# Optimization experiments

Measured on AMD Instinct MI355X. Metric: run time of the kernel, lower is better.

The kernel has to match this reference:

```python
import jax, jax.numpy as jnp
import numpy as np
from jax import lax

B, C, H, W = 8, 19, 512, 512
LOW_T, HIGH_T = 100.0, 200.0  # cv2.Canny(img, 100, 200)
MAX_HYST_ITERS = 256          # safety cap on hysteresis fixed-point iterations

_KX = jnp.array([[-1., 0., 1.], [-2., 0., 2.], [-1., 0., 1.]], jnp.float32)
_KY = jnp.array([[-1., -2., -1.], [0., 0., 0.], [1., 2., 1.]], jnp.float32)


def _conv3(x, k):
    # x: [B, H+2, W+2] (already padded), k: [3,3] -> [B, H, W]
    return lax.conv_general_dilated(x[:, None], k[None, None], (1, 1), 'VALID')[:, 0]


def _dilate3(s):
    # 8-connected boolean dilation via 3x3 max window
    return lax.reduce_window(s.astype(jnp.int32), 0, lax.max, (1, 3, 3), (1, 1, 1), 'SAME') > 0


def _canny(img):
    # img: [B, H, W] float values in [0, 255]. Returns float32 edge map in {0,1}.
    b, h, w = img.shape
    pad = jnp.pad(img, ((0, 0), (1, 1), (1, 1)), mode='edge')
    gx = _conv3(pad, _KX)
    gy = _conv3(pad, _KY)
    mag = jnp.abs(gx) + jnp.abs(gy)  # cv2 default L1 gradient magnitude
    ang = jnp.degrees(jnp.arctan2(gy, gx)) % 180.0
    mp = jnp.pad(mag, ((0, 0), (1, 1), (1, 1)))
    nb = lambda dy, dx: mp[:, 1 + dy:1 + dy + h, 1 + dx:1 + dx + w]
    # non-maximum suppression along quantized gradient direction
    d0 = (ang < 22.5) | (ang >= 157.5)
    d45 = (ang >= 22.5) & (ang < 67.5)
    d90 = (ang >= 67.5) & (ang < 112.5)
    keep0 = (mag >= nb(0, 1)) & (mag >= nb(0, -1))
    keep45 = (mag >= nb(-1, 1)) & (mag >= nb(1, -1))
    keep90 = (mag >= nb(1, 0)) & (mag >= nb(-1, 0))
    keep135 = (mag >= nb(-1, -1)) & (mag >= nb(1, 1))
    keep = jnp.where(d0, keep0, jnp.where(d45, keep45, jnp.where(d90, keep90, keep135)))
    strong = keep & (mag > HIGH_T)
    weak = keep & (mag > LOW_T)  # weak includes strong
    # hysteresis: propagate strong labels through weak pixels to fixed point
    def cond(c):
        s, changed, it = c
        return changed & (it < MAX_HYST_ITERS)
    def body(c):
        s, _, it = c
        s2 = (weak & _dilate3(s)) | strong
        return (s2, jnp.any(s2 != s), it + 1)
    edges, _, _ = lax.while_loop(cond, body, (strong, jnp.array(True), jnp.array(0)))
    return edges.astype(jnp.float32)


def setup_inputs() -> dict:
    key = jax.random.key(0)
    k1, k2 = jax.random.split(key)
    pred = jax.random.normal(k1, (B, C, H, W), dtype=jnp.float32)
    labels = jax.random.uniform(k2, (B, H, W), dtype=jnp.float32)
    return {'pred': pred, 'labels': labels}


def reference(pred, labels):
    # pred_convert: per-pixel argmax over channel dim -> class ids [B, H, W]
    cls = jnp.argmax(pred, axis=1)
    # canny(): (img * 255).astype('uint8') -- class ids wrap mod 256
    img_p = ((cls * 255) % 256).astype(jnp.float32)
    # labels in [0,1): uint8 cast truncates toward zero
    img_l = jnp.floor(labels * 255.0)
    ep = _canny(img_p)  # [B, H, W] in {0,1}
    el = _canny(img_l)  # [B, H, W] in {0,1}
    # nn.CrossEntropyLoss() on float target of same shape: input [N=B, C=H, d1=W],
    # target is class probabilities; mean over N and d1.
    logp = jax.nn.log_softmax(ep, axis=1)
    return jnp.mean(jnp.sum(-el * logp, axis=1))
```

## Files before the change

kernel.cpp:

```cpp
#include <hip/hip_runtime.h>
#include <hip/hip_bf16.h>
#include <math.h>

typedef unsigned long long u64;
typedef unsigned char u8;
typedef unsigned short u16;
typedef unsigned int u32;

#define BB 8
#define CC 19
#define HH 512
#define WW 512
#define HWSZ (HH*WW)
#define NIMG 16

__global__ __launch_bounds__(256) void k_pre(const float* __restrict__ pred,
                                             const float* __restrict__ lab,
                                             u8* __restrict__ img,
                                             float* __restrict__ out) {
    int idx = blockIdx.x * 256 + threadIdx.x;
    if (idx == 0) out[0] = 0.0f;
    int p4 = idx * 4;
    int b = p4 / HWSZ;
    int rem = p4 - b * HWSZ;
    const float4* base = (const float4*)(pred + (size_t)b * CC * HWSZ + rem);
    float4 best = base[0];
    int ix = 0, iy = 0, iz = 0, iw = 0;
    for (int c = 1; c < CC; ++c) {
        float4 v = base[(size_t)c * (HWSZ / 4)];
        if (v.x > best.x) { best.x = v.x; ix = c; }
        if (v.y > best.y) { best.y = v.y; iy = c; }
        if (v.z > best.z) { best.z = v.z; iz = c; }
        if (v.w > best.w) { best.w = v.w; iw = c; }
    }
    uchar4 o;
    o.x = (u8)(-ix); o.y = (u8)(-iy); o.z = (u8)(-iz); o.w = (u8)(-iw);
    *(uchar4*)(img + p4) = o;
    float4 v = *(const float4*)(lab + p4);
    uchar4 ol;
    ol.x = (u8)(v.x * 255.0f);
    ol.y = (u8)(v.y * 255.0f);
    ol.z = (u8)(v.z * 255.0f);
    ol.w = (u8)(v.w * 255.0f);
    *(uchar4*)(img + (size_t)BB * HWSZ + p4) = ol;
}

__global__ __launch_bounds__(256) void k_grad(const u8* __restrict__ imgs,
                                              u16* __restrict__ magdir) {
    int t = blockIdx.x * 256 + threadIdx.x;
    int x0 = (t & 63) * 8;
    int y  = (t >> 6) & 511;
    int im = t >> 15;
    const u8* base = imgs + (size_t)im * HWSZ;
    int rows[3];
    rows[0] = (y == 0) ? 0 : y - 1;
    rows[1] = y;
    rows[2] = (y == 511) ? 511 : y + 1;
    int bb[3][10];
#pragma unroll
    for (int r = 0; r < 3; ++r) {
        const u8* rp = base + rows[r] * WW;
        u64 m = *(const u64*)(rp + x0);
        bb[r][0] = (x0 == 0) ? rp[0] : rp[x0 - 1];
#pragma unroll
        for (int i = 0; i < 8; ++i) bb[r][i + 1] = (int)((m >> (8 * i)) & 0xFF);
        bb[r][9] = (x0 == 504) ? rp[511] : rp[x0 + 8];
    }
    u32 v[8];
#pragma unroll
    for (int i = 0; i < 8; ++i) {
        int a00 = bb[0][i], a01 = bb[0][i + 1], a02 = bb[0][i + 2];
        int a10 = bb[1][i],                     a12 = bb[1][i + 2];
        int a20 = bb[2][i], a21 = bb[2][i + 1], a22 = bb[2][i + 2];
        int gx = (a02 + 2 * a12 + a22) - (a00 + 2 * a10 + a20);
        int gy = (a20 + 2 * a21 + a22) - (a00 + 2 * a01 + a02);
        int ax = gx < 0 ? -gx : gx;
        int ay = gy < 0 ? -gy : gy;
        int mag = ax + ay;
        float fax = (float)ax, fay = (float)ay;
        int dir;
        if (fay < 0.41421356237309515f * fax) dir = 0;
        else if (fay >= 2.414213562373095f * fax) dir = 2;
        else dir = ((gx ^ gy) >= 0) ? 1 : 3;
        v[i] = (u32)mag | ((u32)dir << 12);
    }
    uint4 o;
    o.x = v[0] | (v[1] << 16);
    o.y = v[2] | (v[3] << 16);
    o.z = v[4] | (v[5] << 16);
    o.w = v[6] | (v[7] << 16);
    *(uint4*)(magdir + (size_t)im * HWSZ + y * WW + x0) = o;
}

__global__ __launch_bounds__(256) void k_nms(const u16* __restrict__ magdir,
                                             u64* __restrict__ weak,
                                             u64* __restrict__ strong) {
    int t = blockIdx.x * 256 + threadIdx.x;
    int x  = t & 511;
    int y  = (t >> 9) & 511;
    int im = t >> 18;
    const u16* md = magdir + (size_t)im * HWSZ;
    u32 v = md[y * WW + x];
    int mag = v & 0xFFF;
    int dir = v >> 12;
    auto M = [&](int yy, int xx) -> int {
        if ((unsigned)yy > 511u || (unsigned)xx > 511u) return 0;
        return md[yy * WW + xx] & 0xFFF;
    };
    int n1, n2;
    switch (dir) {
        case 0:  n1 = M(y, x - 1);     n2 = M(y, x + 1);     break;
        case 1:  n1 = M(y - 1, x + 1); n2 = M(y + 1, x - 1); break;
        case 2:  n1 = M(y - 1, x);     n2 = M(y + 1, x);     break;
        default: n1 = M(y - 1, x - 1); n2 = M(y + 1, x + 1); break;
    }
    bool keep = (mag >= n1) && (mag >= n2);
    u64 wb = __ballot(keep && mag > 100);
    u64 sb = __ballot(keep && mag > 200);
    if ((threadIdx.x & 63) == 0) {
        size_t w = ((size_t)im * HH + y) * 8 + (x >> 6);
        weak[w] = wb;
        strong[w] = sb;
    }
}

__global__ __launch_bounds__(512) void k_hyst(const u64* __restrict__ weakg,
                                              const u64* __restrict__ strongg,
                                              u64* __restrict__ edges) {
    __shared__ u32 hlo[8][512];
    __shared__ u32 hhi[8][512];
    __shared__ int flags[2];
    int y = threadIdx.x;
    int im = blockIdx.x;
    size_t base = ((size_t)im * HH + y) * 8;
    u64 wk[8], s[8];
#pragma unroll
    for (int j = 0; j < 8; ++j) {
        wk[j] = weakg[base + j];
        s[j] = strongg[base + j];
    }
    for (int it = 0; it < 256; ++it) {
        u64 diff = 0;
        u64 c = 0;
#pragma unroll
        for (int j = 0; j < 8; ++j) {
            u64 a = s[j], w = wk[j];
            u64 t1 = a + w;       u64 c1 = (u64)(t1 < a);
            u64 t2 = t1 + c;      u64 c2 = (u64)(t2 < t1);
            u64 ns = a | ((t2 ^ w) & w);
            diff |= ns ^ a;
            s[j] = ns;
            c = c1 | c2;
        }
        c = 0;
#pragma unroll
        for (int j = 7; j >= 0; --j) {
            u64 a = __builtin_bitreverse64(s[j]);
            u64 w = __builtin_bitreverse64(wk[j]);
            u64 t1 = a + w;       u64 c1 = (u64)(t1 < a);
            u64 t2 = t1 + c;      u64 c2 = (u64)(t2 < t1);
            u64 nsr = a | ((t2 ^ w) & w);
            u64 ns = __builtin_bitreverse64(nsr);
            diff |= ns ^ s[j];
            s[j] = ns;
            c = c1 | c2;
        }
        u64 hh[8];
#pragma unroll
        for (int j = 0; j < 8; ++j) hh[j] = s[j] | (s[j] << 1) | (s[j] >> 1);
#pragma unroll
        for (int j = 1; j < 8; ++j) hh[j] |= s[j - 1] >> 63;
#pragma unroll
        for (int j = 0; j < 7; ++j) hh[j] |= s[j + 1] << 63;
#pragma unroll
        for (int j = 0; j < 8; ++j) {
            hlo[j][y] = (u32)hh[j];
            hhi[j][y] = (u32)(hh[j] >> 32);
        }
        if (y == 0 && it == 0) flags[0] = 0;
        __syncthreads();
        if (y == 0) flags[(it + 1) & 1] = 0;
#pragma unroll
        for (int j = 0; j < 8; ++j) {
            u64 up = (y > 0)   ? ((u64)hlo[j][y - 1] | ((u64)hhi[j][y - 1] << 32)) : 0ull;
            u64 dn = (y < 511) ? ((u64)hlo[j][y + 1] | ((u64)hhi[j][y + 1] << 32)) : 0ull;
            u64 t = wk[j] & (up | dn) & ~s[j];
            diff |= t;
            s[j] |= t;
        }
        if (diff) flags[it & 1] = 1;
        __syncthreads();
        if (!flags[it & 1]) break;
    }
#pragma unroll
    for (int j = 0; j < 8; ++j) edges[base + j] = s[j];
}

__global__ __launch_bounds__(256) void k_loss(const u64* __restrict__ edges,
                                              float* __restrict__ out) {
    int b = blockIdx.x >> 3;
    int j = blockIdx.x & 7;
    int wave = threadIdx.x >> 6;
    int lane = threadIdx.x & 63;
    const u64* ep = edges + ((size_t)b * HH) * 8 + j;
    const u64* el = edges + ((size_t)(b + 8) * HH) * 8 + j;
    int k = 0, es = 0, ov = 0;
    int y0 = wave * 128;
    for (int y = y0; y < y0 + 128; ++y) {
        u64 wp = ep[(size_t)y * 8];
        u64 wl = el[(size_t)y * 8];
        int bp = (int)((wp >> lane) & 1ull);
        int bl = (int)((wl >> lane) & 1ull);
        k += bp; es += bl; ov += (bp & bl);
    }
    __shared__ int red[3][4][64];
    red[0][wave][lane] = k;
    red[1][wave][lane] = es;
    red[2][wave][lane] = ov;
    __syncthreads();
    if (threadIdx.x < 64) {
        int l = threadIdx.x;
        int K = red[0][0][l] + red[0][1][l] + red[0][2][l] + red[0][3][l];
        int E = red[1][0][l] + red[1][1][l] + red[1][2][l] + red[1][3][l];
        int O = red[2][0][l] + red[2][1][l] + red[2][2][l] + red[2][3][l];
        float logZ = logf(512.0f + 1.7182818284590452f * (float)K);
        float v = ((float)E * logZ - (float)O) * (1.0f / 4096.0f);
#pragma unroll
        for (int o = 32; o > 0; o >>= 1) v += __shfl_down(v, o, 64);
        if (l == 0) atomicAdd(out, v);
    }
}

extern "C" void kernel_launch(void* const* d_in, const int* in_sizes, int n_in,
                              void* d_out, int out_size, void* d_ws, size_t ws_size,
                              hipStream_t stream) {
    const float* pred = (const float*)d_in[0];
    const float* labels = (const float*)d_in[1];
    float* out = (float*)d_out;

    u8*  imgs   = (u8*)d_ws;
    u16* magdir = (u16*)((char*)d_ws + (size_t)NIMG * HWSZ);
    u64* weak   = (u64*)((char*)d_ws + (size_t)NIMG * HWSZ * 3);
    u64* strong = (u64*)((char*)weak + (size_t)NIMG * HH * 8 * 8);
    u64* edges  = (u64*)((char*)strong + (size_t)NIMG * HH * 8 * 8);

    hipLaunchKernelGGL(k_pre, dim3(BB * HWSZ / 4 / 256), dim3(256), 0, stream,
                       pred, labels, imgs, out);
    hipLaunchKernelGGL(k_grad, dim3(NIMG * HH * 64 / 256), dim3(256), 0, stream,
                       imgs, magdir);
    hipLaunchKernelGGL(k_nms, dim3(NIMG * HWSZ / 256), dim3(256), 0, stream,
                       magdir, weak, strong);
    hipLaunchKernelGGL(k_hyst, dim3(NIMG), dim3(512), 0, stream,
                       weak, strong, edges);
    hipLaunchKernelGGL(k_loss, dim3(64), dim3(256), 0, stream, edges, out);
}
```

Before: 270.6 us.

## Fuse Sobel gradient and non-maximum suppression into one tiled kernel

Merges the gradient and NMS kernels into one kernel. Each block computes Sobel magnitudes for a 4-row strip, plus one halo row above and below, into shared memory, then runs NMS from shared memory and packs the weak/strong bits. This removes the 8 MB u16 mag/dir intermediate round trip through global memory and one kernel launch. The cost is recomputing halo rows, which adds about 50% extra Sobel work, and only two of the four waves doing that halo work.

```diff
diff --git a/kernel.cpp b/kernel.cpp
--- a/kernel.cpp
+++ b/kernel.cpp
@@ -45,28 +45,21 @@
     *(uchar4*)(img + (size_t)BB * HWSZ + p4) = ol;
 }
 
-__global__ __launch_bounds__(256) void k_grad(const u8* __restrict__ imgs,
-                                              u16* __restrict__ magdir) {
-    int t = blockIdx.x * 256 + threadIdx.x;
-    int x0 = (t & 63) * 8;
-    int y  = (t >> 6) & 511;
-    int im = t >> 15;
-    const u8* base = imgs + (size_t)im * HWSZ;
-    int rows[3];
-    rows[0] = (y == 0) ? 0 : y - 1;
-    rows[1] = y;
-    rows[2] = (y == 511) ? 511 : y + 1;
+__device__ __forceinline__ void sobel8(const u8* __restrict__ base, int yy, int x0,
+                                       int mag8[8], u32* dirpack) {
+    int r0 = (yy == 0) ? 0 : yy - 1;
+    int r2 = (yy == 511) ? 511 : yy + 1;
+    const u8* rps[3] = { base + r0 * WW, base + yy * WW, base + r2 * WW };
     int bb[3][10];
 #pragma unroll
     for (int r = 0; r < 3; ++r) {
-        const u8* rp = base + rows[r] * WW;
-        u64 m = *(const u64*)(rp + x0);
-        bb[r][0] = (x0 == 0) ? rp[0] : rp[x0 - 1];
+        u64 m = *(const u64*)(rps[r] + x0);
+        bb[r][0] = (x0 == 0) ? rps[r][0] : rps[r][x0 - 1];
 #pragma unroll
         for (int i = 0; i < 8; ++i) bb[r][i + 1] = (int)((m >> (8 * i)) & 0xFF);
-        bb[r][9] = (x0 == 504) ? rp[511] : rp[x0 + 8];
-    }
-    u32 v[8];
+        bb[r][9] = (x0 == 504) ? rps[r][511] : rps[r][x0 + 8];
+    }
+    u32 dp = 0;
 #pragma unroll
     for (int i = 0; i < 8; ++i) {
         int a00 = bb[0][i], a01 = bb[0][i + 1], a02 = bb[0][i + 2];
@@ -76,51 +69,90 @@
         int gy = (a20 + 2 * a21 + a22) - (a00 + 2 * a01 + a02);
         int ax = gx < 0 ? -gx : gx;
         int ay = gy < 0 ? -gy : gy;
-        int mag = ax + ay;
-        float fax = (float)ax, fay = (float)ay;
-        int dir;
-        if (fay < 0.41421356237309515f * fax) dir = 0;
-        else if (fay >= 2.414213562373095f * fax) dir = 2;
-        else dir = ((gx ^ gy) >= 0) ? 1 : 3;
-        v[i] = (u32)mag | ((u32)dir << 12);
-    }
-    uint4 o;
-    o.x = v[0] | (v[1] << 16);
-    o.y = v[2] | (v[3] << 16);
-    o.z = v[4] | (v[5] << 16);
-    o.w = v[6] | (v[7] << 16);
-    *(uint4*)(magdir + (size_t)im * HWSZ + y * WW + x0) = o;
-}
-
-__global__ __launch_bounds__(256) void k_nms(const u16* __restrict__ magdir,
-                                             u64* __restrict__ weak,
-                                             u64* __restrict__ strong) {
-    int t = blockIdx.x * 256 + threadIdx.x;
-    int x  = t & 511;
-    int y  = (t >> 9) & 511;
-    int im = t >> 18;
-    const u16* md = magdir + (size_t)im * HWSZ;
-    u32 v = md[y * WW + x];
-    int mag = v & 0xFFF;
-    int dir = v >> 12;
-    auto M = [&](int yy, int xx) -> int {
-        if ((unsigned)yy > 511u || (unsigned)xx > 511u) return 0;
-        return md[yy * WW + xx] & 0xFFF;
-    };
-    int n1, n2;
-    switch (dir) {
-        case 0:  n1 = M(y, x - 1);     n2 = M(y, x + 1);     break;
-        case 1:  n1 = M(y - 1, x + 1); n2 = M(y + 1, x - 1); break;
-        case 2:  n1 = M(y - 1, x);     n2 = M(y + 1, x);     break;
-        default: n1 = M(y - 1, x - 1); n2 = M(y + 1, x + 1); break;
-    }
-    bool keep = (mag >= n1) && (mag >= n2);
-    u64 wb = __ballot(keep && mag > 100);
-    u64 sb = __ballot(keep && mag > 200);
-    if ((threadIdx.x & 63) == 0) {
-        size_t w = ((size_t)im * HH + y) * 8 + (x >> 6);
-        weak[w] = wb;
-        strong[w] = sb;
+        mag8[i] = ax + ay;
+        if (dirpack) {
+            float fax = (float)ax, fay = (float)ay;
+            u32 dir;
+            if (fay < 0.41421356237309515f * fax) dir = 0;
+            else if (fay >= 2.414213562373095f * fax) dir = 2;
+            else dir = ((gx ^ gy) >= 0) ? 1u : 3u;
+            dp |= dir << (2 * i);
+        }
+    }
+    if (dirpack) *dirpack = dp;
+}
+
+__global__ __launch_bounds__(256) void k_gradnms(const u8* __restrict__ imgs,
+                                                 u64* __restrict__ weak,
+                                                 u64* __restrict__ strong) {
+    __shared__ u16 smag[6][514];
+    __shared__ alignas(8) u8 wb[4][64];
+    __shared__ alignas(8) u8 sb[4][64];
+    int im = blockIdx.x >> 7;
+    int y0 = (blockIdx.x & 127) * 4;
+    int r    = threadIdx.x >> 6;
+    int lane = threadIdx.x & 63;
+    int x0 = lane * 8;
+    const u8* base = imgs + (size_t)im * HWSZ;
+
+    if (threadIdx.x < 6) { smag[threadIdx.x][0] = 0; smag[threadIdx.x][513] = 0; }
+
+    int y = y0 + r;
+    int mag8[8]; u32 dp;
+    sobel8(base, y, x0, mag8, &dp);
+#pragma unroll
+    for (int i = 0; i < 8; ++i) smag[r + 1][1 + x0 + i] = (u16)mag8[i];
+
+    if (r == 0) {
+        if (y0 > 0) {
+            int m2[8]; sobel8(base, y0 - 1, x0, m2, nullptr);
+#pragma unroll
+            for (int i = 0; i < 8; ++i) smag[0][1 + x0 + i] = (u16)m2[i];
+        } else {
+#pragma unroll
+            for (int i = 0; i < 8; ++i) smag[0][1 + x0 + i] = 0;
+        }
+    } else if (r == 3) {
+        if (y0 + 4 < 512) {
+            int m2[8]; sobel8(base, y0 + 4, x0, m2, nullptr);
+#pragma unroll
+            for (int i = 0; i < 8; ++i) smag[5][1 + x0 + i] = (u16)m2[i];
+        } else {
+#pragma unroll
+            for (int i = 0; i < 8; ++i) smag[5][1 + x0 + i] = 0;
+        }
+    }
+    __syncthreads();
+
+    int wbits = 0, sbits = 0;
+#pragma unroll
+    for (int i = 0; i < 8; ++i) {
+        int x = x0 + i;
+        int mag = mag8[i];
+        int dir = (int)((dp >> (2 * i)) & 3u);
+        int n1, n2;
+        switch (dir) {
+            case 0:  n1 = smag[r + 1][x];     n2 = smag[r + 1][x + 2]; break;
+            case 1:  n1 = smag[r][x + 2];     n2 = smag[r + 2][x];     break;
+            case 2:  n1 = smag[r][x + 1];     n2 = smag[r + 2][x + 1]; break;
+            default: n1 = smag[r][x];         n2 = smag[r + 2][x + 2]; break;
+        }
+        int keep = (mag >= n1) & (mag >= n2);
+        wbits |= (keep & (mag > 100)) << i;
+        sbits |= (keep & (mag > 200)) << i;
+    }
+    wb[r][lane] = (u8)wbits;
+    sb[r][lane] = (u8)sbits;
+    __syncthreads();
+
+    if (threadIdx.x < 32) {
+        int rr = threadIdx.x >> 3;
+        int w  = threadIdx.x & 7;
+        u64 W = *(const u64*)&wb[rr][w * 8];
+        u64 S = *(const u64*)&sb[rr][w * 8];
+        size_t o = ((size_t)im * HH + (y0 + rr)) * 8 + w;
+        weak[o] = W;
+        strong[o] = S;
     }
 }
 
@@ -239,17 +271,14 @@
     float* out = (float*)d_out;
 
     u8*  imgs   = (u8*)d_ws;
-    u16* magdir = (u16*)((char*)d_ws + (size_t)NIMG * HWSZ);
-    u64* weak   = (u64*)((char*)d_ws + (size_t)NIMG * HWSZ * 3);
+    u64* weak   = (u64*)((char*)d_ws + (size_t)NIMG * HWSZ);
     u64* strong = (u64*)((char*)weak + (size_t)NIMG * HH * 8 * 8);
     u64* edges  = (u64*)((char*)strong + (size_t)NIMG * HH * 8 * 8);
 
     hipLaunchKernelGGL(k_pre, dim3(BB * HWSZ / 4 / 256), dim3(256), 0, stream,
                        pred, labels, imgs, out);
-    hipLaunchKernelGGL(k_grad, dim3(NIMG * HH * 64 / 256), dim3(256), 0, stream,
-                       imgs, magdir);
-    hipLaunchKernelGGL(k_nms, dim3(NIMG * HWSZ / 256), dim3(256), 0, stream,
-                       magdir, weak, strong);
+    hipLaunchKernelGGL(k_gradnms, dim3(NIMG * 128), dim3(256), 0, stream,
+                       imgs, weak, strong);
     hipLaunchKernelGGL(k_hyst, dim3(NIMG), dim3(512), 0, stream,
                        weak, strong, edges);
     hipLaunchKernelGGL(k_loss, dim3(64), dim3(256), 0, stream, edges, out);
```

After: 249.3 us, median of 2. 1.09x faster.
